# Optimization experiments

Hardware: AMD Instinct MI355X
Metric: run time of the kernel (lower is better)

## Reference

```python
import jax, jax.numpy as jnp
import numpy as np

# ---- static config (mirrors PaCoVoxelLoss init) ----
NUM_QUERIES = 20
FACTOR = 64
NUM_GT = 12
K_NEIGHBORS = 8          # repulsion.num_neighbors
REP_EPS = 1e-12          # repulsion.epsilon
BANDWIDTH = 0.03         # repulsion.kernel_bandwidth
RADIUS = 0.07            # repulsion.radius
ALPHA_PARAM = 0.5
BETA_CHAMFER = 20.0
W_CLS, W_REP, W_CH1, W_CH2 = 1.0, 1.0, 1.0, 1.0
PAD_COST = 1e6           # pad value to square the rectangular assignment problem


def _hungarian(cost):
    # Jonker-Volgenant / e-maxx shortest augmenting path; cost: (n, n) float64.
    # Returns col_to_row: for each column j, the row assigned to it.
    n = cost.shape[0]
    INF = 1e18
    u = np.zeros(n + 1); v = np.zeros(n + 1)
    p = np.zeros(n + 1, dtype=np.int64)
    way = np.zeros(n + 1, dtype=np.int64)
    for i in range(1, n + 1):
        p[0] = i; j0 = 0
        minv = np.full(n + 1, INF)
        used = np.zeros(n + 1, dtype=bool)
        while True:
            used[j0] = True
            i0 = p[j0]; delta = INF; j1 = 0
            for j in range(1, n + 1):
                if not used[j]:
                    cur = cost[i0 - 1, j - 1] - u[i0] - v[j]
                    if cur < minv[j]:
                        minv[j] = cur; way[j] = j0
                    if minv[j] < delta:
                        delta = minv[j]; j1 = j
            for j in range(n + 1):
                if used[j]:
                    u[p[j]] += delta; v[j] -= delta
                else:
                    minv[j] -= delta
            j0 = j1
            if p[j0] == 0:
                break
        while j0 != 0:
            j1 = way[j0]; p[j0] = p[j1]; j0 = j1
    return p[1:] - 1


def _match(cost_np):
    # cost_np: (B, Q, P) with P <= Q -> rows (B, P): pred row matched to each gt col.
    Bn, Qn, Pn = cost_np.shape
    rows = np.zeros((Bn, Pn), dtype=np.int64)
    for b in range(Bn):
        sq = np.full((Qn, Qn), PAD_COST, dtype=np.float64)
        sq[:, :Pn] = cost_np[b].astype(np.float64)
        rows[b] = _hungarian(sq)[:Pn]
    return rows


def _gather_q(A, rows):
    # A: (B, Q, P), rows: (B, P) -> A[b, rows[b,p], p] : (B, P)
    return jnp.take_along_axis(A, rows[:, None, :], axis=1)[:, 0, :]


def _bce_logits(x, t):
    return jnp.maximum(x, 0.0) - x * t + jnp.log1p(jnp.exp(-jnp.abs(x)))


def _cost_terms(pred_normals, pred_distances, gt_normals, gt_distances, points, gt_masks):
    mask_f = gt_masks.astype(points.dtype)           # (B, P, N)
    cnt = mask_f.sum(-1)                             # (B, P)
    # |points . n_q - d_q| for all query planes: (B, Q, N)
    pp = jnp.abs(jnp.einsum('bnd,bqd->bqn', points, pred_normals) - pred_distances[:, :, None])
    cham_raw = jnp.einsum('bqn,bpn->bqp', pp, mask_f) / jnp.maximum(cnt, 1.0)[:, None, :]
    has = (cnt > 0)[:, None, :]                      # (B, 1, P)
    normal_sim = 1.0 - jnp.abs(jnp.einsum('bqd,bpd->bqp', pred_normals, gt_normals))
    dist_diff = jnp.abs(pred_distances[:, :, None] - gt_distances[:, None, :])
    cost = normal_sim + 0.5 * dist_diff + 5.0 * jnp.where(has, cham_raw, 1.0)
    return cost, cham_raw, normal_sim, dist_diff, has


def _losses(pred_logits, pred_normals, pred_distances, gt_normals, gt_distances,
            points, reconstructed_points, gt, gt_masks, rows):
    _, cham_raw, normal_sim, dist_diff, has = _cost_terms(
        pred_normals, pred_distances, gt_normals, gt_distances, points, gt_masks)

    # classification loss: target 1 at matched pred rows
    Qn = pred_logits.shape[1]
    cls_target = jax.nn.one_hot(rows, Qn, dtype=pred_logits.dtype).sum(axis=1)  # (B, Q)
    cls_loss = _bce_logits(pred_logits, cls_target).mean()

    # param loss over matched pairs (mean over P matches, mean over B)
    param_loss = (_gather_q(normal_sim, rows).mean(-1) + _gather_q(dist_diff, rows).mean(-1)).mean()

    # pvd chamfer: point-to-plane term, zero for empty masks, /P /B
    pvd_chamfer = _gather_q(jnp.where(has, cham_raw, 0.0), rows).mean()

    # repulsion loss on per-query point groups
    Bn = reconstructed_points.shape[0]
    rp = reconstructed_points.reshape(Bn, NUM_QUERIES, FACTOR, 3)
    d2 = jnp.sum((rp[:, :, :, None, :] - rp[:, :, None, :, :]) ** 2, axis=-1)  # (B,Q,F,F)
    _, idx = jax.lax.top_k(-d2, K_NEIGHBORS)       # k nearest incl. self
    dn = jnp.maximum(jnp.take_along_axis(d2, idx[..., 1:], axis=-1), REP_EPS)  # (B,Q,F,k-1)
    w = jnp.exp(-dn / BANDWIDTH ** 2)
    rep = jnp.maximum(jnp.mean((RADIUS - jnp.sqrt(dn)) * w, axis=(2, 3)), 0.0).mean()

    # fine-grained chamfer (L1 and L2) between reconstructed and gt clouds
    diff = reconstructed_points[:, :, None, :] - gt[:, None, :, :]  # (B, M, G, 3)
    d1 = jnp.abs(diff).sum(-1)
    d2c = (diff ** 2).sum(-1)
    ch1 = (0.5 * (d1.min(axis=2).mean(axis=1) + d1.min(axis=1).mean(axis=1))).mean()
    ch2 = (0.5 * (d2c.min(axis=2).mean(axis=1) + d2c.min(axis=1).mean(axis=1))).mean()

    total = (W_CLS * cls_loss + ALPHA_PARAM * param_loss + BETA_CHAMFER * pvd_chamfer
             + W_REP * rep + W_CH1 * ch1 + W_CH2 * ch2)
    return total


def setup_inputs() -> dict:
    key = jax.random.key(0)
    ks = jax.random.split(key, 10)
    B, Q, P, N, G = 8, NUM_QUERIES, NUM_GT, 4096, 2048

    def unit(k, shape):
        v = jax.random.normal(k, shape, dtype=jnp.float32)
        return v / jnp.linalg.norm(v, axis=-1, keepdims=True)

    return {
        'pred_logits': jax.random.normal(ks[0], (B, Q), dtype=jnp.float32),
        'pred_normals': unit(ks[1], (B, Q, 3)),
        'pred_distances': jax.random.normal(ks[2], (B, Q), dtype=jnp.float32),
        'gt_normals': unit(ks[3], (B, P, 3)),
        'gt_distances': jax.random.normal(ks[4], (B, P), dtype=jnp.float32),
        'gt_masks': jax.random.bernoulli(ks[5], 0.3, (B, P, N)),
        'points': jax.random.normal(ks[6], (B, N, 3), dtype=jnp.float32),
        'reconstructed_points': 0.5 * jax.random.normal(ks[7], (B, Q * FACTOR, 3), dtype=jnp.float32),
        'gt': jax.random.normal(ks[8], (B, G, 3), dtype=jnp.float32),
        'gt_index': jax.random.randint(ks[9], (B, G), 0, P, dtype=jnp.int64) if jax.config.jax_enable_x64 else jax.random.randint(ks[9], (B, G), 0, P, dtype=jnp.int32),
    }


def reference(pred_logits, pred_normals, pred_distances, gt_normals, gt_distances,
              points, reconstructed_points, gt, gt_masks, gt_index):
    cost = _cost_terms(pred_normals, pred_distances, gt_normals, gt_distances, points, gt_masks)[0]
    rows = jnp.asarray(_match(np.asarray(cost)))  # Hungarian (host, like scipy in original)
    return _losses(pred_logits, pred_normals, pred_distances, gt_normals, gt_distances,
                   points, reconstructed_points, gt, gt_masks, rows)
```

## Files before the change

### kernel.cpp

```cpp
#include <hip/hip_runtime.h>
#include <math.h>

#define Bn 8
#define Qn 20
#define Pn 12
#define Nn 4096
#define Gn 2048
#define Mn 1280
#define Fn 64
#define KNB 7
#define NCOST 160
#define NCHA 160
#define NCHB 256
#define NREP 20
#define NBLK 596
#define C2_TARGET 425
#define SCOPE_AGENT __HIP_MEMORY_SCOPE_AGENT


__device__ __forceinline__ void ast(float* p, float v) {
    __hip_atomic_store(p, v, __ATOMIC_RELAXED, SCOPE_AGENT);
}
__device__ __forceinline__ float ald(const float* p) {
    return __hip_atomic_load(p, __ATOMIC_RELAXED, SCOPE_AGENT);
}

__device__ __forceinline__ int rdlane_i(int v, int l) {
    return __builtin_amdgcn_readlane(v, l);
}
__device__ __forceinline__ float rdlane_f(float v, int l) {
    return __int_as_float(__builtin_amdgcn_readlane(__float_as_int(v), l));
}
__device__ __forceinline__ unsigned wave_min_u32(unsigned x) {
    unsigned t;
    t = (unsigned)__builtin_amdgcn_update_dpp((int)0xFFFFFFFF, (int)x, 0x111, 0xF, 0xF, false);
    x = t < x ? t : x;
    t = (unsigned)__builtin_amdgcn_update_dpp((int)0xFFFFFFFF, (int)x, 0x112, 0xF, 0xF, false);
    x = t < x ? t : x;
    t = (unsigned)__builtin_amdgcn_update_dpp((int)0xFFFFFFFF, (int)x, 0x114, 0xF, 0xF, false);
    x = t < x ? t : x;
    t = (unsigned)__builtin_amdgcn_update_dpp((int)0xFFFFFFFF, (int)x, 0x118, 0xF, 0xF, false);
    x = t < x ? t : x;
    t = (unsigned)__builtin_amdgcn_update_dpp((int)0xFFFFFFFF, (int)x, 0x142, 0xF, 0xF, false);
    x = t < x ? t : x;
    t = (unsigned)__builtin_amdgcn_update_dpp((int)0xFFFFFFFF, (int)x, 0x143, 0xF, 0xF, false);
    x = t < x ? t : x;
    return x;
}

__device__ __forceinline__ void bump_c2(float* ws, float* out, unsigned init) {
    unsigned* c2P = (unsigned*)(ws + 7936);
    unsigned old = __hip_atomic_fetch_add(c2P, 1u, __ATOMIC_ACQ_REL, SCOPE_AGENT);
    if (old - init == (unsigned)(C2_TARGET - 1)) {
        float a0 = 0.f, a1 = 0.f, a2 = 0.f, a4 = 0.f, a5 = 0.f;
#pragma unroll
        for (int b = 0; b < 8; ++b) {
            a0 += ald(ws + 8000 + 16 * b + 0);
            a1 += ald(ws + 8000 + 16 * b + 1);
            a2 += ald(ws + 8000 + 16 * b + 2);
        }
#pragma unroll 8
        for (int c = 0; c < NCHA; ++c) {
            a4 += ald(ws + 8192 + 16 * c + 0);
            a5 += ald(ws + 8192 + 16 * c + 1);
        }
#pragma unroll 8
        for (int c = 0; c < NCHB; ++c) {
            a4 += ald(ws + 10752 + 16 * c + 0);
            a5 += ald(ws + 10752 + 16 * c + 1);
        }
        float a3 = ald(ws + 7952);
        out[0] = a0 + 0.5f * a1 + 20.f * a2 + a3 + a4 + a5;
        unsigned* w = (unsigned*)ws;
        __hip_atomic_store(&w[7936], init, __ATOMIC_RELAXED, SCOPE_AGENT);
        __hip_atomic_store(&w[7968], init, __ATOMIC_RELAXED, SCOPE_AGENT);
#pragma unroll
        for (int b = 0; b < 8; ++b)
            __hip_atomic_store(&w[7808 + 16 * b], init, __ATOMIC_RELAXED, SCOPE_AGENT);
    }
}

__global__ __launch_bounds__(512, 2)
void fused_kernel(const float* __restrict__ pred_logits,
                  const float* __restrict__ pred_normals,
                  const float* __restrict__ pred_distances,
                  const float* __restrict__ gt_normals,
                  const float* __restrict__ gt_distances,
                  const float* __restrict__ points,
                  const int*   __restrict__ gt_masks,
                  const float* __restrict__ recon,
                  const float* __restrict__ gt,
                  float* __restrict__ ws,
                  float* __restrict__ out) {
    __shared__ __align__(16) float smem[8192];
    __shared__ int sflag;
    const int blk = blockIdx.x;
    const int tid = threadIdx.x;

    float* cham = ws;
    float* ns   = ws + 1920;
    float* dd   = ws + 3840;
    float* cost = ws + 5760;
    float* cnt  = ws + 7680;
    unsigned* baseP = (unsigned*)(ws + 7783);
    unsigned* repcP = (unsigned*)(ws + 7968);
    float* rep_part = ws + 14848;

    const unsigned init = __hip_atomic_load(baseP, __ATOMIC_RELAXED, SCOPE_AGENT);

    if (blk < NCOST) {
        const int b = blk & 7, q = blk >> 3;
        const float nx = pred_normals[(b * Qn + q) * 3 + 0];
        const float ny = pred_normals[(b * Qn + q) * 3 + 1];
        const float nz = pred_normals[(b * Qn + q) * 3 + 2];
        const float dq = pred_distances[b * Qn + q];

        if (tid < 256) {
            float accs[Pn], accw[Pn];
#pragma unroll
            for (int p = 0; p < Pn; ++p) { accs[p] = 0.f; accw[p] = 0.f; }
            const float* ptb = points + (size_t)b * Nn * 3;
            const int*   mb  = gt_masks + (size_t)b * Pn * Nn;
            for (int n = tid; n < Nn; n += 256) {
                float px = ptb[n * 3 + 0], py = ptb[n * 3 + 1], pz = ptb[n * 3 + 2];
                float pp = fabsf(px * nx + py * ny + pz * nz - dq);
#pragma unroll
                for (int p = 0; p < Pn; ++p) {
                    float m = (float)mb[(size_t)p * Nn + n];
                    accs[p] += pp * m;
                    accw[p] += m;
                }
            }
#pragma unroll
            for (int p = 0; p < Pn; ++p) {
                smem[p * 256 + tid] = accs[p];
                smem[(p + Pn) * 256 + tid] = accw[p];
            }
        }
        __syncthreads();
        for (int off = 128; off > 0; off >>= 1) {
            if (tid < off) {
#pragma unroll
                for (int r = 0; r < 2 * Pn; ++r) smem[r * 256 + tid] += smem[r * 256 + tid + off];
            }
            __syncthreads();
        }
        if (tid < Pn) {
            const int p = tid;
            float c  = smem[(p + Pn) * 256];
            float cv = smem[p * 256] / fmaxf(c, 1.f);
            float gnx = gt_normals[(b * Pn + p) * 3 + 0];
            float gny = gt_normals[(b * Pn + p) * 3 + 1];
            float gnz = gt_normals[(b * Pn + p) * 3 + 2];
            float nsim = 1.f - fabsf(nx * gnx + ny * gny + nz * gnz);
            float ddv  = fabsf(dq - gt_distances[b * Pn + p]);
            int idx = (b * Qn + q) * Pn + p;
            ast(&cham[idx], cv);
            ast(&ns[idx],   nsim);
            ast(&dd[idx],   ddv);
            ast(&cost[idx], nsim + 0.5f * ddv + 5.f * ((c > 0.f) ? cv : 1.f));
            if (q == 0) ast(&cnt[b * Pn + p], c);
        }
        __syncthreads();
        if (tid == 0)
            __hip_atomic_fetch_add((unsigned*)(ws + 7808 + 16 * b), 1u,
                                   __ATOMIC_RELEASE, SCOPE_AGENT);
        if (blk >= 8) return;

        if (tid == 0) {
            unsigned* dB = (unsigned*)(ws + 7808 + 16 * blk);
            while (__hip_atomic_load(dB, __ATOMIC_RELAXED, SCOPE_AGENT) - init != 20u)
                __builtin_amdgcn_s_sleep(2);
            (void)__hip_atomic_load(dB, __ATOMIC_ACQUIRE, SCOPE_AGENT);
        }
        __syncthreads();

        if (tid < 64) {
            const int b2 = blk;
            const int t = tid;
            const int col = t;
            const bool isCol = (col >= 1 && col <= Qn);

            float cr[Pn];
#pragma unroll
            for (int k = 0; k < Pn; ++k) cr[k] = 0.f;
            if (isCol) {
                const float* cb = cost + ((size_t)b2 * Qn + (col - 1)) * Pn;
#pragma unroll
                for (int k = 0; k < Pn; ++k) cr[k] = ald(&cb[k]);
            }

            float v = 0.f, u = 0.f, minv = 0.f;
            int way = 0, p = 0;

            for (int i = 1; i <= Pn; ++i) {
                minv = 1e30f;
                bool used = false;
                bool rowInPath = false;
                int j0s = 0;
                while (true) {
                    if (col == j0s) used = true;
                    int i0s = (j0s == 0) ? i : rdlane_i(p, j0s);
                    if (t == i0s) rowInPath = true;
                    float u_i0 = rdlane_f(u, i0s);
                    const int bs = i0s - 1;
                    float l10 = (bs & 1) ? cr[1]  : cr[0];
                    float l11 = (bs & 1) ? cr[3]  : cr[2];
                    float l12 = (bs & 1) ? cr[5]  : cr[4];
                    float l13 = (bs & 1) ? cr[7]  : cr[6];
                    float l14 = (bs & 1) ? cr[9]  : cr[8];
                    float l15 = (bs & 1) ? cr[11] : cr[10];
                    float l20 = (bs & 2) ? l11 : l10;
                    float l21 = (bs & 2) ? l13 : l12;
                    float l22 = (bs & 2) ? l15 : l14;
                    float cij = (bs >= 8) ? l22 : ((bs >= 4) ? l21 : l20);
                    if (isCol && !used) {
                        float cur = cij - u_i0 - v;
                        if (cur < minv) { minv = cur; way = j0s; }
                    }
                    float mv = (isCol && !used) ? minv : 1e30f;
                    unsigned kb = __float_as_uint(mv);
                    kb = ((int)kb < 0) ? ~kb : (kb | 0x80000000u);
                    kb = (kb & ~31u) | (unsigned)(col & 31);
                    unsigned kmin = (unsigned)rdlane_i((int)wave_min_u32(kb), 63);
                    int j1 = (int)(kmin & 31u);
                    float delta = rdlane_f(minv, j1);
                    if (used || col == 0) v -= delta;
                    else if (isCol)       minv -= delta;
                    if (rowInPath)        u += delta;
                    j0s = j1;
                    int pj0 = rdlane_i(p, j0s);
                    if (pj0 == 0) break;
                }
                while (j0s != 0) {
                    int wj = rdlane_i(way, j0s);
                    int pw = (wj == 0) ? i : rdlane_i(p, wj);
                    if (col == j0s) p = pw;
                    j0s = wj;
                }
            }

            float cls = 0.f, par = 0.f, pvd = 0.f;
            if (isCol) {
                float x = pred_logits[b2 * Qn + (col - 1)];
                float tgt = (p > 0) ? 1.f : 0.f;
                cls = fmaxf(x, 0.f) - x * tgt + log1pf(expf(-fabsf(x)));
                if (p > 0) {
                    int idx = (b2 * Qn + (col - 1)) * Pn + (p - 1);
                    par = ald(&ns[idx]) + ald(&dd[idx]);
                    pvd = (ald(&cnt[b2 * Pn + (p - 1)]) > 0.f) ? ald(&cham[idx]) : 0.f;
                }
            }
            for (int off = 32; off > 0; off >>= 1) {
                cls += __shfl_down(cls, off);
                par += __shfl_down(par, off);
                pvd += __shfl_down(pvd, off);
            }
            if (t == 0) {
                float* slot = ws + 8000 + 16 * b2;
                ast(slot + 0, cls / (float)(Bn * Qn));
                ast(slot + 1, par / (float)(Bn * Pn));
                ast(slot + 2, pvd / (float)(Bn * Pn));
                bump_c2(ws, out, init);
            }
        }
        return;
    } else if (blk < NCOST + NCHA + NCHB) {
        const int a0 = blk - NCOST;
        const bool isA = (a0 < NCHA);
        int chunk;
        if (isA) { int r = a0;        chunk = (r & 7) * 20 + (r >> 3); }
        else     { int r = a0 - NCHA; chunk = (r & 7) * 32 + (r >> 3); }
        const int lt = tid & 63;
        const int part = tid >> 6;
        const int idx = chunk * 64 + lt;
        const float* inner;
        const float* op;
        int ninner;
        float scale;
        float* slot;
        if (isA) {
            const int b = idx / Mn;
            inner = gt + (size_t)b * Gn * 3;
            op = recon + (size_t)idx * 3;
            ninner = Gn;
            scale = 0.5f / (float)(Bn * Mn);
            slot = ws + 8192 + 16 * chunk;
        } else {
            const int b = idx / Gn;
            inner = recon + (size_t)b * Mn * 3;
            op = gt + (size_t)idx * 3;
            ninner = Mn;
            scale = 0.5f / (float)(Bn * Gn);
            slot = ws + 10752 + 16 * chunk;
        }
        float4* tile = reinterpret_cast<float4*>(smem);
        for (int j = tid; j < ninner; j += 512) {
            const float* ip = inner + j * 3;
            float4 tv;
            tv.x = ip[0]; tv.y = ip[1]; tv.z = ip[2]; tv.w = 0.f;
            tile[j] = tv;
        }
        __syncthreads();
        const float x = op[0], y = op[1], z = op[2];
        const int span = ninner >> 3;
        const int j0 = part * span, j1 = j0 + span;
        float m1 = 3.4e38f, m2 = 3.4e38f;
#pragma unroll 4
        for (int j = j0; j < j1; ++j) {
            float4 tv = tile[j];
            float dx = x - tv.x, dy = y - tv.y, dz = z - tv.z;
            float d1 = fabsf(dx) + fabsf(dy) + fabsf(dz);
            float d2 = dx * dx + dy * dy + dz * dz;
            m1 = fminf(m1, d1); m2 = fminf(m2, d2);
        }
        __syncthreads();
        float* s1 = smem;
        float* s2 = smem + 512;
        s1[tid] = m1;
        s2[tid] = m2;
        __syncthreads();
        float* t1 = smem + 1024;
        float* t2 = smem + 1088;
        if (tid < 64) {
            float M1 = s1[tid], M2 = s2[tid];
#pragma unroll
            for (int pp = 1; pp < 8; ++pp) {
                M1 = fminf(M1, s1[pp * 64 + tid]);
                M2 = fminf(M2, s2[pp * 64 + tid]);
            }
            t1[tid] = M1 * scale;
            t2[tid] = M2 * scale;
        }
        __syncthreads();
        for (int off = 32; off > 0; off >>= 1) {
            if (tid < off) { t1[tid] += t1[tid + off]; t2[tid] += t2[tid + off]; }
            __syncthreads();
        }
        if (tid == 0) {
            ast(slot + 0, t1[0]);
            ast(slot + 1, t2[0]);
            bump_c2(ws, out, init);
        }
        return;
    }

    {
        const int wave = tid >> 6, lane = tid & 63;
        const int g = (blk - (NCOST + NCHA + NCHB)) * 8 + wave;
        float* xs = smem + wave * 192;
        float* ys = xs + 64;
        float* zs = xs + 128;
        const float* base = recon + (size_t)g * Fn * 3;
        xs[lane] = base[lane * 3 + 0];
        ys[lane] = base[lane * 3 + 1];
        zs[lane] = base[lane * 3 + 2];
        float best[KNB];
#pragma unroll
        for (int k = 0; k < KNB; ++k) best[k] = 3.4e38f;
        const float xi = xs[lane], yi = ys[lane], zi = zs[lane];
        for (int j = 0; j < Fn; ++j) {
            float dx = xi - xs[j], dy = yi - ys[j], dz = zi - zs[j];
            float d2 = dx * dx + dy * dy + dz * dz;
            d2 = (j == lane) ? 3.4e38f : d2;
#pragma unroll
            for (int k = 0; k < KNB; ++k) {
                float lo = fminf(best[k], d2);
                float hi = fmaxf(best[k], d2);
                best[k] = lo;
                d2 = hi;
            }
        }
        float sum = 0.f;
#pragma unroll
        for (int k = 0; k < KNB; ++k) {
            float dn = fmaxf(best[k], 1e-12f);
            float w  = expf(-dn / (0.03f * 0.03f));
            sum += (0.07f - sqrtf(dn)) * w;
        }
        for (int off = 32; off > 0; off >>= 1) sum += __shfl_down(sum, off);
        if (lane == 0) ast(&rep_part[g], fmaxf(sum / (float)(Fn * KNB), 0.f));
        __syncthreads();
        if (tid == 0) {
            unsigned old = __hip_atomic_fetch_add(repcP, 1u, __ATOMIC_ACQ_REL, SCOPE_AGENT);
            sflag = (old - init == (unsigned)(NREP - 1)) ? 1 : 0;
        }
        __syncthreads();
        if (sflag) {
            float* s1 = smem + 2048;
            if (tid < 256)
                s1[tid] = (tid < Bn * Qn) ? ald(&rep_part[tid]) / (float)(Bn * Qn) : 0.f;
            __syncthreads();
            for (int off = 128; off > 0; off >>= 1) {
                if (tid < off) s1[tid] += s1[tid + off];
                __syncthreads();
            }
            if (tid == 0) {
                ast(ws + 7952, s1[0]);
                bump_c2(ws, out, init);
            }
        }
    }
}

extern "C" void kernel_launch(void* const* d_in, const int* in_sizes, int n_in,
                              void* d_out, int out_size, void* d_ws, size_t ws_size,
                              hipStream_t stream) {
    const float* pred_logits    = (const float*)d_in[0];
    const float* pred_normals   = (const float*)d_in[1];
    const float* pred_distances = (const float*)d_in[2];
    const float* gt_normals     = (const float*)d_in[3];
    const float* gt_distances   = (const float*)d_in[4];
    const int*   gt_masks       = (const int*)d_in[5];
    const float* points         = (const float*)d_in[6];
    const float* recon          = (const float*)d_in[7];
    const float* gt             = (const float*)d_in[8];

    fused_kernel<<<NBLK, 512, 0, stream>>>(pred_logits, pred_normals, pred_distances,
                                           gt_normals, gt_distances, points, gt_masks,
                                           recon, gt, (float*)d_ws, (float*)d_out);
}
```

Baseline: 120.1 us.

## Hierarchize completion counter and parallelize final assembly loads across threads

Replaces the single global completion counter that all 425 finishing blocks bumped with per-batch sub-counters for the chamfer blocks. Only the last chamfer block of each group bumps the global counter, so the global target drops to 17. The final reduction now loads all partials in parallel across the block into shared memory before thread 0 sums them, instead of thread 0 issuing ~850 serial atomic loads. This adds an extra atomic per chamfer block and more __syncthreads, and the new per-group counters must be reset for reuse.

New measurement: 110.4 us. -8.1%, faster.

```diff
diff --git a/kernel.cpp b/kernel.cpp
--- a/kernel.cpp
+++ b/kernel.cpp
@@ -14,7 +14,7 @@
 #define NCHB 256
 #define NREP 20
 #define NBLK 596
-#define C2_TARGET 425
+#define C2_TARGET 17
 #define SCOPE_AGENT __HIP_MEMORY_SCOPE_AGENT
 
 
@@ -48,35 +48,58 @@
     return x;
 }
 
-__device__ __forceinline__ void bump_c2(float* ws, float* out, unsigned init) {
+__device__ __forceinline__ bool bump_c2(float* ws, unsigned init) {
     unsigned* c2P = (unsigned*)(ws + 7936);
     unsigned old = __hip_atomic_fetch_add(c2P, 1u, __ATOMIC_ACQ_REL, SCOPE_AGENT);
-    if (old - init == (unsigned)(C2_TARGET - 1)) {
+    return (old - init == (unsigned)(C2_TARGET - 1));
+}
+
+__device__ __forceinline__ void assemble(float* ws, float* out, unsigned init,
+                                         float* ld, int tid) {
+    if (tid < 8) {
+        ld[3 * tid + 0] = ald(ws + 8000 + 16 * tid + 0);
+        ld[3 * tid + 1] = ald(ws + 8000 + 16 * tid + 1);
+        ld[3 * tid + 2] = ald(ws + 8000 + 16 * tid + 2);
+    } else if (tid < 168) {
+        int c = tid - 8;
+        ld[24 + 2 * c + 0] = ald(ws + 8192 + 16 * c + 0);
+        ld[24 + 2 * c + 1] = ald(ws + 8192 + 16 * c + 1);
+    } else if (tid < 424) {
+        int c = tid - 168;
+        ld[344 + 2 * c + 0] = ald(ws + 10752 + 16 * c + 0);
+        ld[344 + 2 * c + 1] = ald(ws + 10752 + 16 * c + 1);
+    } else if (tid == 424) {
+        ld[856] = ald(ws + 7952);
+    }
+    __syncthreads();
+    if (tid == 0) {
         float a0 = 0.f, a1 = 0.f, a2 = 0.f, a4 = 0.f, a5 = 0.f;
 #pragma unroll
         for (int b = 0; b < 8; ++b) {
-            a0 += ald(ws + 8000 + 16 * b + 0);
-            a1 += ald(ws + 8000 + 16 * b + 1);
-            a2 += ald(ws + 8000 + 16 * b + 2);
+            a0 += ld[3 * b + 0];
+            a1 += ld[3 * b + 1];
+            a2 += ld[3 * b + 2];
         }
 #pragma unroll 8
         for (int c = 0; c < NCHA; ++c) {
-            a4 += ald(ws + 8192 + 16 * c + 0);
-            a5 += ald(ws + 8192 + 16 * c + 1);
+            a4 += ld[24 + 2 * c + 0];
+            a5 += ld[24 + 2 * c + 1];
         }
 #pragma unroll 8
         for (int c = 0; c < NCHB; ++c) {
-            a4 += ald(ws + 10752 + 16 * c + 0);
-            a5 += ald(ws + 10752 + 16 * c + 1);
-        }
-        float a3 = ald(ws + 7952);
+            a4 += ld[344 + 2 * c + 0];
+            a5 += ld[344 + 2 * c + 1];
+        }
+        float a3 = ld[856];
         out[0] = a0 + 0.5f * a1 + 20.f * a2 + a3 + a4 + a5;
         unsigned* w = (unsigned*)ws;
         __hip_atomic_store(&w[7936], init, __ATOMIC_RELAXED, SCOPE_AGENT);
         __hip_atomic_store(&w[7968], init, __ATOMIC_RELAXED, SCOPE_AGENT);
 #pragma unroll
-        for (int b = 0; b < 8; ++b)
+        for (int b = 0; b < 8; ++b) {
             __hip_atomic_store(&w[7808 + 16 * b], init, __ATOMIC_RELAXED, SCOPE_AGENT);
+            __hip_atomic_store(&w[15360 + 16 * b], init, __ATOMIC_RELAXED, SCOPE_AGENT);
+        }
     }
 }
 
@@ -94,8 +117,10 @@
                   float* __restrict__ out) {
     __shared__ __align__(16) float smem[8192];
     __shared__ int sflag;
+    __shared__ int fflag;
     const int blk = blockIdx.x;
     const int tid = threadIdx.x;
+    float* const ld = smem + 4096;
 
     float* cham = ws;
     float* ns   = ws + 1920;
@@ -261,9 +286,11 @@
                 ast(slot + 0, cls / (float)(Bn * Qn));
                 ast(slot + 1, par / (float)(Bn * Pn));
                 ast(slot + 2, pvd / (float)(Bn * Pn));
-                bump_c2(ws, out, init);
-            }
-        }
+                fflag = bump_c2(ws, init) ? 1 : 0;
+            }
+        }
+        __syncthreads();
+        if (fflag) assemble(ws, out, init, ld, tid);
         return;
     } else if (blk < NCOST + NCHA + NCHB) {
         const int a0 = blk - NCOST;
@@ -340,8 +367,14 @@
         if (tid == 0) {
             ast(slot + 0, t1[0]);
             ast(slot + 1, t2[0]);
-            bump_c2(ws, out, init);
-        }
+            unsigned* l1 = (unsigned*)(ws + 15360 + 16 * (blk & 7));
+            unsigned old = __hip_atomic_fetch_add(l1, 1u, __ATOMIC_ACQ_REL, SCOPE_AGENT);
+            int last = 0;
+            if (old - init == 51u) last = bump_c2(ws, init) ? 1 : 0;
+            fflag = last;
+        }
+        __syncthreads();
+        if (fflag) assemble(ws, out, init, ld, tid);
         return;
     }
 
@@ -384,6 +417,7 @@
         if (tid == 0) {
             unsigned old = __hip_atomic_fetch_add(repcP, 1u, __ATOMIC_ACQ_REL, SCOPE_AGENT);
             sflag = (old - init == (unsigned)(NREP - 1)) ? 1 : 0;
+            fflag = 0;
         }
         __syncthreads();
         if (sflag) {
@@ -397,9 +431,11 @@
             }
             if (tid == 0) {
                 ast(ws + 7952, s1[0]);
-                bump_c2(ws, out, init);
-            }
-        }
+                fflag = bump_c2(ws, init) ? 1 : 0;
+            }
+        }
+        __syncthreads();
+        if (fflag) assemble(ws, out, init, ld, tid);
     }
 }
 
```

## Split fused kernel into compute kernel plus single-block Hungarian/reduction kernel

Applied to the files above, without the earlier changes.

Replaces the single persistent kernel, which used atomic counters, spin-waits and last-block-done reductions, with two launches. The first kernel computes cost terms, chamfer partials and repulsion partials using plain stores. A second single-block kernel runs the eight Hungarian matchings in parallel, one per wave, and does the final reduction. This removes the spin-wait and the serialized atomic last-block logic, at the cost of an extra kernel launch and an inter-kernel gap.

Measured after the change: 110.5 us. 1.09x faster.

```diff
diff --git a/kernel.cpp b/kernel.cpp
--- a/kernel.cpp
+++ b/kernel.cpp
@@ -13,17 +13,8 @@
 #define NCHA 160
 #define NCHB 256
 #define NREP 20
-#define NBLK 596
-#define C2_TARGET 425
-#define SCOPE_AGENT __HIP_MEMORY_SCOPE_AGENT
-
-
-__device__ __forceinline__ void ast(float* p, float v) {
-    __hip_atomic_store(p, v, __ATOMIC_RELAXED, SCOPE_AGENT);
-}
-__device__ __forceinline__ float ald(const float* p) {
-    return __hip_atomic_load(p, __ATOMIC_RELAXED, SCOPE_AGENT);
-}
+#define NBLK1 596
+
 
 __device__ __forceinline__ int rdlane_i(int v, int l) {
     return __builtin_amdgcn_readlane(v, l);
@@ -48,52 +39,17 @@
     return x;
 }
 
-__device__ __forceinline__ void bump_c2(float* ws, float* out, unsigned init) {
-    unsigned* c2P = (unsigned*)(ws + 7936);
-    unsigned old = __hip_atomic_fetch_add(c2P, 1u, __ATOMIC_ACQ_REL, SCOPE_AGENT);
-    if (old - init == (unsigned)(C2_TARGET - 1)) {
-        float a0 = 0.f, a1 = 0.f, a2 = 0.f, a4 = 0.f, a5 = 0.f;
-#pragma unroll
-        for (int b = 0; b < 8; ++b) {
-            a0 += ald(ws + 8000 + 16 * b + 0);
-            a1 += ald(ws + 8000 + 16 * b + 1);
-            a2 += ald(ws + 8000 + 16 * b + 2);
-        }
-#pragma unroll 8
-        for (int c = 0; c < NCHA; ++c) {
-            a4 += ald(ws + 8192 + 16 * c + 0);
-            a5 += ald(ws + 8192 + 16 * c + 1);
-        }
-#pragma unroll 8
-        for (int c = 0; c < NCHB; ++c) {
-            a4 += ald(ws + 10752 + 16 * c + 0);
-            a5 += ald(ws + 10752 + 16 * c + 1);
-        }
-        float a3 = ald(ws + 7952);
-        out[0] = a0 + 0.5f * a1 + 20.f * a2 + a3 + a4 + a5;
-        unsigned* w = (unsigned*)ws;
-        __hip_atomic_store(&w[7936], init, __ATOMIC_RELAXED, SCOPE_AGENT);
-        __hip_atomic_store(&w[7968], init, __ATOMIC_RELAXED, SCOPE_AGENT);
-#pragma unroll
-        for (int b = 0; b < 8; ++b)
-            __hip_atomic_store(&w[7808 + 16 * b], init, __ATOMIC_RELAXED, SCOPE_AGENT);
-    }
-}
-
 __global__ __launch_bounds__(512, 2)
-void fused_kernel(const float* __restrict__ pred_logits,
-                  const float* __restrict__ pred_normals,
-                  const float* __restrict__ pred_distances,
-                  const float* __restrict__ gt_normals,
-                  const float* __restrict__ gt_distances,
-                  const float* __restrict__ points,
-                  const int*   __restrict__ gt_masks,
-                  const float* __restrict__ recon,
-                  const float* __restrict__ gt,
-                  float* __restrict__ ws,
-                  float* __restrict__ out) {
+void k1_kernel(const float* __restrict__ pred_normals,
+               const float* __restrict__ pred_distances,
+               const float* __restrict__ gt_normals,
+               const float* __restrict__ gt_distances,
+               const float* __restrict__ points,
+               const int*   __restrict__ gt_masks,
+               const float* __restrict__ recon,
+               const float* __restrict__ gt,
+               float* __restrict__ ws) {
     __shared__ __align__(16) float smem[8192];
-    __shared__ int sflag;
     const int blk = blockIdx.x;
     const int tid = threadIdx.x;
 
@@ -102,11 +58,9 @@
     float* dd   = ws + 3840;
     float* cost = ws + 5760;
     float* cnt  = ws + 7680;
-    unsigned* baseP = (unsigned*)(ws + 7783);
-    unsigned* repcP = (unsigned*)(ws + 7968);
-    float* rep_part = ws + 14848;
-
-    const unsigned init = __hip_atomic_load(baseP, __ATOMIC_RELAXED, SCOPE_AGENT);
+    float* slotA = ws + 8192;
+    float* slotB = ws + 8512;
+    float* rep_part = ws + 9024;
 
     if (blk < NCOST) {
         const int b = blk & 7, q = blk >> 3;
@@ -155,114 +109,11 @@
             float nsim = 1.f - fabsf(nx * gnx + ny * gny + nz * gnz);
             float ddv  = fabsf(dq - gt_distances[b * Pn + p]);
             int idx = (b * Qn + q) * Pn + p;
-            ast(&cham[idx], cv);
-            ast(&ns[idx],   nsim);
-            ast(&dd[idx],   ddv);
-            ast(&cost[idx], nsim + 0.5f * ddv + 5.f * ((c > 0.f) ? cv : 1.f));
-            if (q == 0) ast(&cnt[b * Pn + p], c);
-        }
-        __syncthreads();
-        if (tid == 0)
-            __hip_atomic_fetch_add((unsigned*)(ws + 7808 + 16 * b), 1u,
-                                   __ATOMIC_RELEASE, SCOPE_AGENT);
-        if (blk >= 8) return;
-
-        if (tid == 0) {
-            unsigned* dB = (unsigned*)(ws + 7808 + 16 * blk);
-            while (__hip_atomic_load(dB, __ATOMIC_RELAXED, SCOPE_AGENT) - init != 20u)
-                __builtin_amdgcn_s_sleep(2);
-            (void)__hip_atomic_load(dB, __ATOMIC_ACQUIRE, SCOPE_AGENT);
-        }
-        __syncthreads();
-
-        if (tid < 64) {
-            const int b2 = blk;
-            const int t = tid;
-            const int col = t;
-            const bool isCol = (col >= 1 && col <= Qn);
-
-            float cr[Pn];
-#pragma unroll
-            for (int k = 0; k < Pn; ++k) cr[k] = 0.f;
-            if (isCol) {
-                const float* cb = cost + ((size_t)b2 * Qn + (col - 1)) * Pn;
-#pragma unroll
-                for (int k = 0; k < Pn; ++k) cr[k] = ald(&cb[k]);
-            }
-
-            float v = 0.f, u = 0.f, minv = 0.f;
-            int way = 0, p = 0;
-
-            for (int i = 1; i <= Pn; ++i) {
-                minv = 1e30f;
-                bool used = false;
-                bool rowInPath = false;
-                int j0s = 0;
-                while (true) {
-                    if (col == j0s) used = true;
-                    int i0s = (j0s == 0) ? i : rdlane_i(p, j0s);
-                    if (t == i0s) rowInPath = true;
-                    float u_i0 = rdlane_f(u, i0s);
-                    const int bs = i0s - 1;
-                    float l10 = (bs & 1) ? cr[1]  : cr[0];
-                    float l11 = (bs & 1) ? cr[3]  : cr[2];
-                    float l12 = (bs & 1) ? cr[5]  : cr[4];
-                    float l13 = (bs & 1) ? cr[7]  : cr[6];
-                    float l14 = (bs & 1) ? cr[9]  : cr[8];
-                    float l15 = (bs & 1) ? cr[11] : cr[10];
-                    float l20 = (bs & 2) ? l11 : l10;
-                    float l21 = (bs & 2) ? l13 : l12;
-                    float l22 = (bs & 2) ? l15 : l14;
-                    float cij = (bs >= 8) ? l22 : ((bs >= 4) ? l21 : l20);
-                    if (isCol && !used) {
-                        float cur = cij - u_i0 - v;
-                        if (cur < minv) { minv = cur; way = j0s; }
-                    }
-                    float mv = (isCol && !used) ? minv : 1e30f;
-                    unsigned kb = __float_as_uint(mv);
-                    kb = ((int)kb < 0) ? ~kb : (kb | 0x80000000u);
-                    kb = (kb & ~31u) | (unsigned)(col & 31);
-                    unsigned kmin = (unsigned)rdlane_i((int)wave_min_u32(kb), 63);
-                    int j1 = (int)(kmin & 31u);
-                    float delta = rdlane_f(minv, j1);
-                    if (used || col == 0) v -= delta;
-                    else if (isCol)       minv -= delta;
-                    if (rowInPath)        u += delta;
-                    j0s = j1;
-                    int pj0 = rdlane_i(p, j0s);
-                    if (pj0 == 0) break;
-                }
-                while (j0s != 0) {
-                    int wj = rdlane_i(way, j0s);
-                    int pw = (wj == 0) ? i : rdlane_i(p, wj);
-                    if (col == j0s) p = pw;
-                    j0s = wj;
-                }
-            }
-
-            float cls = 0.f, par = 0.f, pvd = 0.f;
-            if (isCol) {
-                float x = pred_logits[b2 * Qn + (col - 1)];
-                float tgt = (p > 0) ? 1.f : 0.f;
-                cls = fmaxf(x, 0.f) - x * tgt + log1pf(expf(-fabsf(x)));
-                if (p > 0) {
-                    int idx = (b2 * Qn + (col - 1)) * Pn + (p - 1);
-                    par = ald(&ns[idx]) + ald(&dd[idx]);
-                    pvd = (ald(&cnt[b2 * Pn + (p - 1)]) > 0.f) ? ald(&cham[idx]) : 0.f;
-                }
-            }
-            for (int off = 32; off > 0; off >>= 1) {
-                cls += __shfl_down(cls, off);
-                par += __shfl_down(par, off);
-                pvd += __shfl_down(pvd, off);
-            }
-            if (t == 0) {
-                float* slot = ws + 8000 + 16 * b2;
-                ast(slot + 0, cls / (float)(Bn * Qn));
-                ast(slot + 1, par / (float)(Bn * Pn));
-                ast(slot + 2, pvd / (float)(Bn * Pn));
-                bump_c2(ws, out, init);
-            }
+            cham[idx] = cv;
+            ns[idx]   = nsim;
+            dd[idx]   = ddv;
+            cost[idx] = nsim + 0.5f * ddv + 5.f * ((c > 0.f) ? cv : 1.f);
+            if (q == 0) cnt[b * Pn + p] = c;
         }
         return;
     } else if (blk < NCOST + NCHA + NCHB) {
@@ -285,14 +136,14 @@
             op = recon + (size_t)idx * 3;
             ninner = Gn;
             scale = 0.5f / (float)(Bn * Mn);
-            slot = ws + 8192 + 16 * chunk;
+            slot = slotA + 2 * chunk;
         } else {
             const int b = idx / Gn;
             inner = recon + (size_t)b * Mn * 3;
             op = gt + (size_t)idx * 3;
             ninner = Mn;
             scale = 0.5f / (float)(Bn * Gn);
-            slot = ws + 10752 + 16 * chunk;
+            slot = slotB + 2 * chunk;
         }
         float4* tile = reinterpret_cast<float4*>(smem);
         for (int j = tid; j < ninner; j += 512) {
@@ -338,9 +189,8 @@
             __syncthreads();
         }
         if (tid == 0) {
-            ast(slot + 0, t1[0]);
-            ast(slot + 1, t2[0]);
-            bump_c2(ws, out, init);
+            slot[0] = t1[0];
+            slot[1] = t2[0];
         }
         return;
     }
@@ -379,27 +229,145 @@
             sum += (0.07f - sqrtf(dn)) * w;
         }
         for (int off = 32; off > 0; off >>= 1) sum += __shfl_down(sum, off);
-        if (lane == 0) ast(&rep_part[g], fmaxf(sum / (float)(Fn * KNB), 0.f));
-        __syncthreads();
-        if (tid == 0) {
-            unsigned old = __hip_atomic_fetch_add(repcP, 1u, __ATOMIC_ACQ_REL, SCOPE_AGENT);
-            sflag = (old - init == (unsigned)(NREP - 1)) ? 1 : 0;
-        }
-        __syncthreads();
-        if (sflag) {
-            float* s1 = smem + 2048;
-            if (tid < 256)
-                s1[tid] = (tid < Bn * Qn) ? ald(&rep_part[tid]) / (float)(Bn * Qn) : 0.f;
-            __syncthreads();
-            for (int off = 128; off > 0; off >>= 1) {
-                if (tid < off) s1[tid] += s1[tid + off];
-                __syncthreads();
-            }
-            if (tid == 0) {
-                ast(ws + 7952, s1[0]);
-                bump_c2(ws, out, init);
-            }
-        }
+        if (lane == 0) rep_part[g] = fmaxf(sum / (float)(Fn * KNB), 0.f);
+    }
+}
+
+__global__ void k2_kernel(const float* __restrict__ pred_logits,
+                          const float* __restrict__ ws,
+                          float* __restrict__ out) {
+    __shared__ float sjv[24];
+    __shared__ float sA[320];
+    __shared__ float sB[512];
+    __shared__ float sR[256];
+    const int tid = threadIdx.x;
+    const int t = tid & 63;
+    const int b2 = tid >> 6;
+
+    const float* cham = ws;
+    const float* ns   = ws + 1920;
+    const float* dd   = ws + 3840;
+    const float* cost = ws + 5760;
+    const float* cnt  = ws + 7680;
+    const float* slotA = ws + 8192;
+    const float* slotB = ws + 8512;
+    const float* rep_part = ws + 9024;
+
+    {
+        const int col = t;
+        const bool isCol = (col >= 1 && col <= Qn);
+
+        float cr[Pn];
+#pragma unroll
+        for (int k = 0; k < Pn; ++k) cr[k] = 0.f;
+        if (isCol) {
+            const float* cb = cost + ((size_t)b2 * Qn + (col - 1)) * Pn;
+#pragma unroll
+            for (int k = 0; k < Pn; ++k) cr[k] = cb[k];
+        }
+
+        float v = 0.f, u = 0.f, minv = 0.f;
+        int way = 0, p = 0;
+
+        for (int i = 1; i <= Pn; ++i) {
+            minv = 1e30f;
+            bool used = false;
+            bool rowInPath = false;
+            int j0s = 0;
+            while (true) {
+                if (col == j0s) used = true;
+                int i0s = (j0s == 0) ? i : rdlane_i(p, j0s);
+                if (t == i0s) rowInPath = true;
+                float u_i0 = rdlane_f(u, i0s);
+                const int bs = i0s - 1;
+                float l10 = (bs & 1) ? cr[1]  : cr[0];
+                float l11 = (bs & 1) ? cr[3]  : cr[2];
+                float l12 = (bs & 1) ? cr[5]  : cr[4];
+                float l13 = (bs & 1) ? cr[7]  : cr[6];
+                float l14 = (bs & 1) ? cr[9]  : cr[8];
+                float l15 = (bs & 1) ? cr[11] : cr[10];
+                float l20 = (bs & 2) ? l11 : l10;
+                float l21 = (bs & 2) ? l13 : l12;
+                float l22 = (bs & 2) ? l15 : l14;
+                float cij = (bs >= 8) ? l22 : ((bs >= 4) ? l21 : l20);
+                if (isCol && !used) {
+                    float cur = cij - u_i0 - v;
+                    if (cur < minv) { minv = cur; way = j0s; }
+                }
+                float mv = (isCol && !used) ? minv : 1e30f;
+                unsigned kb = __float_as_uint(mv);
+                kb = ((int)kb < 0) ? ~kb : (kb | 0x80000000u);
+                kb = (kb & ~31u) | (unsigned)(col & 31);
+                unsigned kmin = (unsigned)rdlane_i((int)wave_min_u32(kb), 63);
+                int j1 = (int)(kmin & 31u);
+                float delta = rdlane_f(minv, j1);
+                if (used || col == 0) v -= delta;
+                else if (isCol)       minv -= delta;
+                if (rowInPath)        u += delta;
+                j0s = j1;
+                int pj0 = rdlane_i(p, j0s);
+                if (pj0 == 0) break;
+            }
+            while (j0s != 0) {
+                int wj = rdlane_i(way, j0s);
+                int pw = (wj == 0) ? i : rdlane_i(p, wj);
+                if (col == j0s) p = pw;
+                j0s = wj;
+            }
+        }
+
+        float cls = 0.f, par = 0.f, pvd = 0.f;
+        if (isCol) {
+            float x = pred_logits[b2 * Qn + (col - 1)];
+            float tgt = (p > 0) ? 1.f : 0.f;
+            cls = fmaxf(x, 0.f) - x * tgt + log1pf(expf(-fabsf(x)));
+            if (p > 0) {
+                int idx = (b2 * Qn + (col - 1)) * Pn + (p - 1);
+                par = ns[idx] + dd[idx];
+                pvd = (cnt[b2 * Pn + (p - 1)] > 0.f) ? cham[idx] : 0.f;
+            }
+        }
+        for (int off = 32; off > 0; off >>= 1) {
+            cls += __shfl_down(cls, off);
+            par += __shfl_down(par, off);
+            pvd += __shfl_down(pvd, off);
+        }
+        if (t == 0) {
+            sjv[3 * b2 + 0] = cls / (float)(Bn * Qn);
+            sjv[3 * b2 + 1] = par / (float)(Bn * Pn);
+            sjv[3 * b2 + 2] = pvd / (float)(Bn * Pn);
+        }
+    }
+
+    if (tid < 320) sA[tid] = slotA[tid];
+    if (tid < 512) sB[tid] = slotB[tid];
+    if (tid < 256) sR[tid] = (tid < Bn * Qn) ? rep_part[tid] / (float)(Bn * Qn) : 0.f;
+    __syncthreads();
+    for (int off = 128; off > 0; off >>= 1) {
+        if (tid < off) sR[tid] += sR[tid + off];
+        __syncthreads();
+    }
+
+    if (tid == 0) {
+        float a0 = 0.f, a1 = 0.f, a2 = 0.f, a4 = 0.f, a5 = 0.f;
+#pragma unroll
+        for (int b = 0; b < 8; ++b) {
+            a0 += sjv[3 * b + 0];
+            a1 += sjv[3 * b + 1];
+            a2 += sjv[3 * b + 2];
+        }
+#pragma unroll 8
+        for (int c = 0; c < NCHA; ++c) {
+            a4 += sA[2 * c + 0];
+            a5 += sA[2 * c + 1];
+        }
+#pragma unroll 8
+        for (int c = 0; c < NCHB; ++c) {
+            a4 += sB[2 * c + 0];
+            a5 += sB[2 * c + 1];
+        }
+        float a3 = sR[0];
+        out[0] = a0 + 0.5f * a1 + 20.f * a2 + a3 + a4 + a5;
     }
 }
 
@@ -416,7 +384,8 @@
     const float* recon          = (const float*)d_in[7];
     const float* gt             = (const float*)d_in[8];
 
-    fused_kernel<<<NBLK, 512, 0, stream>>>(pred_logits, pred_normals, pred_distances,
-                                           gt_normals, gt_distances, points, gt_masks,
-                                           recon, gt, (float*)d_ws, (float*)d_out);
-}
+    k1_kernel<<<NBLK1, 512, 0, stream>>>(pred_normals, pred_distances, gt_normals,
+                                         gt_distances, points, gt_masks, recon, gt,
+                                         (float*)d_ws);
+    k2_kernel<<<1, 512, 0, stream>>>(pred_logits, (const float*)d_ws, (float*)d_out);
+}
```
